# Optimization experiments

Measured on AMD Instinct MI355X. Metric: run time of the kernel, lower is better.

Reference implementation:

```python
import jax, jax.numpy as jnp
import numpy as np

K = 128
NITER = 10


def _sq_dist(x, c):
    x2 = jnp.sum(x * x, axis=1, keepdims=True)          # [N,1]
    c2 = jnp.sum(c * c, axis=1)                          # [K]
    return x2 + c2[None, :] - 2.0 * (x @ c.T)


def _kmeans(x, key):
    N, D = x.shape
    idx = jax.random.permutation(key, N)[:K]             # torch.randperm(N)[:K]
    c0 = x[idx]

    def step(c, _):
        cl = jnp.argmin(_sq_dist(x, c), axis=1)          # nearest assignment [N]
        counts = jax.ops.segment_sum(jnp.ones((N,), x.dtype), cl, num_segments=K)  # bincount
        sums = jax.ops.segment_sum(x, cl, num_segments=K)                          # [K,D] (vectorized over D)
        # c = sums / counts; NaN (empty cluster, 0/0) -> 0, matching c[isnan(c)]=0
        c_new = jnp.where(counts[:, None] > 0, sums / jnp.maximum(counts, 1.0)[:, None], 0.0)
        return c_new, None

    c, _ = jax.lax.scan(step, c0, None, length=NITER)
    return c


def setup_inputs() -> dict:
    key = jax.random.key(0)
    x = jax.random.normal(key, (500000, 64), dtype=jnp.float32)
    return {"x": x}


def reference(x):
    # KMeans runs on x.detach(); forward output has no grad path through centroids
    centroids = _kmeans(jax.lax.stop_gradient(x), jax.random.key(42))
    distances = _sq_dist(x, centroids)                   # [N, K]
    # Faithful to normalize_distance: distances.sum(1, keepdim=True)[0] indexes
    # ROW 0 of the [N,1] row-sums -> a single scalar broadcast to all rows.
    denom = jnp.sum(distances[0])
    probs = 1.0 - distances / denom
    return probs
```

## Files before the change

kernel.cpp:

```cpp
#include <hip/hip_runtime.h>
#include <cstdint>
#include <cstddef>

#define NPTS 500000
#define DIM 64
#define KC 128
#define KM_ITERS 10
#define NGROUPS (NPTS / 32)
#define NITERS8 ((NGROUPS + 7) / 8)

typedef __bf16 bf16x8 __attribute__((ext_vector_type(8)));
typedef float f32x4 __attribute__((ext_vector_type(4)));

__device__ __forceinline__ float wave_reduce_add(float v) {
#pragma unroll
  for (int off = 32; off > 0; off >>= 1) v += __shfl_xor(v, off, 64);
  return v;
}

__device__ __forceinline__ bf16x8 cvt8(float4 a, float4 b) {
  bf16x8 r;
  r[0] = (__bf16)a.x; r[1] = (__bf16)a.y; r[2] = (__bf16)a.z; r[3] = (__bf16)a.w;
  r[4] = (__bf16)b.x; r[5] = (__bf16)b.y; r[6] = (__bf16)b.z; r[7] = (__bf16)b.w;
  return r;
}

__global__ void k_initc(const float* __restrict__ x, float* __restrict__ cent,
                        float* __restrict__ c2, float* __restrict__ S,
                        float* __restrict__ CNT) {
  int k = blockIdx.x, d = threadIdx.x;
  long src = (long)k * 3891 + 7;
  float v = x[src * DIM + d];
  cent[k * DIM + d] = v;
#pragma unroll
  for (int p = 0; p < KM_ITERS; p++) S[p * (KC * DIM) + k * DIM + d] = 0.f;
  if (d < KM_ITERS) CNT[d * KC + k] = 0.f;
  float s = wave_reduce_add(v * v);
  if (d == 0) c2[k] = s;
}

__global__ void k_update(const float* __restrict__ sums, const float* __restrict__ cnts,
                         float* __restrict__ cent, float* __restrict__ c2) {
  int k = blockIdx.x, d = threadIdx.x;
  float c = cnts[k];
  float v = (c > 0.f) ? (sums[k * DIM + d] / c) : 0.f;
  cent[k * DIM + d] = v;
  float s = wave_reduce_add(v * v);
  if (d == 0) c2[k] = s;
}

#define DIST_H(V0, V1, MK)                                                     \
  {                                                                            \
    f32x4 acc_[8];                                                             \
    _Pragma("unroll") for (int tt = 0; tt < 8; tt++)                           \
      acc_[tt] = (f32x4){c2h[tt * 4 + 0], c2h[tt * 4 + 1],                     \
                         c2h[tt * 4 + 2], c2h[tt * 4 + 3]};                    \
    _Pragma("unroll") for (int tt = 0; tt < 8; tt++)                           \
      acc_[tt] = __builtin_amdgcn_mfma_f32_16x16x32_bf16(afr0[tt], V0, acc_[tt], 0, 0, 0); \
    _Pragma("unroll") for (int tt = 0; tt < 8; tt++)                           \
      acc_[tt] = __builtin_amdgcn_mfma_f32_16x16x32_bf16(afr1[tt], V1, acc_[tt], 0, 0, 0); \
    float tv[32]; int ti[32];                                                  \
    _Pragma("unroll") for (int i_ = 0; i_ < 32; i_++) {                        \
      tv[i_] = acc_[i_ >> 2][i_ & 3]; ti[i_] = i_;                             \
    }                                                                          \
    _Pragma("unroll") for (int s_ = 16; s_ >= 1; s_ >>= 1)                     \
      _Pragma("unroll") for (int i_ = 0; i_ < s_; i_++) {                      \
        bool t_ = tv[i_ + s_] > tv[i_];                                        \
        tv[i_] = t_ ? tv[i_ + s_] : tv[i_];                                    \
        ti[i_] = t_ ? ti[i_ + s_] : ti[i_];                                    \
      }                                                                        \
    float maxv = tv[0];                                                        \
    int mk = ((ti[0] >> 2) << 4) + grp * 4 + (ti[0] & 3);                      \
    _Pragma("unroll") for (int off = 16; off <= 32; off <<= 1) {               \
      float ov = __shfl_xor(maxv, off, 64);                                    \
      int ok = __shfl_xor(mk, off, 64);                                        \
      if (ov > maxv || (ov == maxv && ok < mk)) { maxv = ov; mk = ok; }        \
    }                                                                          \
    MK = mk;                                                                   \
  }

#define XT_WRITE(XTW, V0, V1, H)                                               \
  {                                                                            \
    int slotb = (((((H) << 1) | (col >> 3)) ^ grp) & 3) * 16 + (col & 7) * 2;  \
    _Pragma("unroll") for (int j = 0; j < 8; j++) {                            \
      *(__bf16*)((XTW) + (grp * 8 + j) * 80 + slotb) = V0[j];                  \
      *(__bf16*)((XTW) + (32 + grp * 8 + j) * 80 + slotb) = V1[j];             \
    }                                                                          \
  }

#define SSQ16(F0, F1, G0, G1)                                                  \
  ((F0.x * F0.x + F0.y * F0.y + F0.z * F0.z + F0.w * F0.w) +                   \
   (F1.x * F1.x + F1.y * F1.y + F1.z * F1.z + F1.w * F1.w) +                   \
   (G0.x * G0.x + G0.y * G0.y + G0.z * G0.z + G0.w * G0.w) +                   \
   (G1.x * G1.x + G1.y * G1.y + G1.z * G1.z + G1.w * G1.w))

template <int FIRST>
__global__ __launch_bounds__(256, 2)
void k_assign(const float* __restrict__ xf, const __bf16* __restrict__ xb,
              __bf16* __restrict__ xbw, const float* __restrict__ cent,
              const float* __restrict__ c2, const float* __restrict__ s_prev,
              const float* __restrict__ cnt_prev, float* __restrict__ s_out,
              float* __restrict__ cnt_out) {
  __shared__ char xT[8][5120];
  __shared__ int sm[8][32];
  __shared__ float lc[KC];
  __shared__ float lcnt[KC];
  __shared__ float lc2[KC];

  const int lane = threadIdx.x & 63;
  const int wid = threadIdx.x >> 6;
  const int col = lane & 15;
  const int grp = lane >> 4;

  bf16x8 afr0[8], afr1[8];
  float c2h[32];

  if constexpr (FIRST) {
    for (int i = threadIdx.x; i < KC; i += 256) lc[i] = 0.f;
#pragma unroll
    for (int t = 0; t < 8; t++) {
      const float* cp = cent + (size_t)(t * 16 + col) * DIM;
      afr0[t] = cvt8(*(const float4*)(cp + grp * 8), *(const float4*)(cp + grp * 8 + 4));
      afr1[t] = cvt8(*(const float4*)(cp + 32 + grp * 8), *(const float4*)(cp + 32 + grp * 8 + 4));
#pragma unroll
      for (int r = 0; r < 4; r++) c2h[t * 4 + r] = -0.5f * c2[t * 16 + grp * 4 + r];
    }
    __syncthreads();
  } else {
    for (int i = threadIdx.x; i < KC; i += 256) { lcnt[i] = cnt_prev[i]; lc[i] = 0.f; }
    __syncthreads();
    float ssq[8];
#pragma unroll
    for (int t = 0; t < 8; t++) {
      int row = t * 16 + col;
      float c = lcnt[row];
      float inv = (c > 0.f) ? 1.f / c : 0.f;
      const float* sp = s_prev + (size_t)row * DIM;
      float4 f0 = *(const float4*)(sp + grp * 8);
      float4 f1 = *(const float4*)(sp + grp * 8 + 4);
      float4 g0 = *(const float4*)(sp + 32 + grp * 8);
      float4 g1 = *(const float4*)(sp + 32 + grp * 8 + 4);
      f0.x *= inv; f0.y *= inv; f0.z *= inv; f0.w *= inv;
      f1.x *= inv; f1.y *= inv; f1.z *= inv; f1.w *= inv;
      g0.x *= inv; g0.y *= inv; g0.z *= inv; g0.w *= inv;
      g1.x *= inv; g1.y *= inv; g1.z *= inv; g1.w *= inv;
      afr0[t] = cvt8(f0, f1);
      afr1[t] = cvt8(g0, g1);
      ssq[t] = SSQ16(f0, f1, g0, g1);
    }
#pragma unroll
    for (int t = 0; t < 8; t++) {
      float s = ssq[t];
      s += __shfl_xor(s, 16, 64);
      s += __shfl_xor(s, 32, 64);
      if (lane < 16 && wid == 0) lc2[t * 16 + col] = s;
    }
    __syncthreads();
#pragma unroll
    for (int t = 0; t < 8; t++)
#pragma unroll
      for (int r = 0; r < 4; r++) c2h[t * 4 + r] = -0.5f * lc2[t * 16 + grp * 4 + r];
  }
#pragma unroll
  for (int t = 0; t < 8; t++) asm volatile("" : "+v"(afr0[t]), "+v"(afr1[t]));
#pragma unroll
  for (int i = 0; i < 32; i++) asm volatile("" : "+v"(c2h[i]));

  f32x4 accs[8];
#pragma unroll
  for (int i = 0; i < 8; i++) accs[i] = (f32x4){0.f, 0.f, 0.f, 0.f};

  const int kbase = wid * 32;

  bf16x8 p0a, p1a, p0b, p1b;
  if constexpr (!FIRST) {
    int g0 = blockIdx.x * 8 + wid * 2;
    if (blockIdx.x < NITERS8 && g0 < NGROUPS) {
      const bf16x8* xr = (const bf16x8*)(xb + (size_t)(g0 * 32 + col) * DIM + grp * 8);
      p0a = xr[0]; p1a = xr[4]; p0b = xr[128]; p1b = xr[132];
    }
  }

  for (int it = blockIdx.x; it < NITERS8; it += gridDim.x) {
    int g0 = it * 8 + wid * 2, g1 = g0 + 1;
    bool e0 = g0 < NGROUPS, e1 = g1 < NGROUPS;

    bf16x8 v0a, v1a, v0b, v1b, w0a, w1a, w0b, w1b;
    if constexpr (FIRST) {
      if (e0) {
        const float* xp = xf + (size_t)(g0 * 32 + col) * DIM + grp * 8;
        const float* xq = xp + 16 * DIM;
        v0a = cvt8(*(const float4*)xp, *(const float4*)(xp + 4));
        v1a = cvt8(*(const float4*)(xp + 32), *(const float4*)(xp + 36));
        v0b = cvt8(*(const float4*)xq, *(const float4*)(xq + 4));
        v1b = cvt8(*(const float4*)(xq + 32), *(const float4*)(xq + 36));
        bf16x8* wp = (bf16x8*)(xbw + (size_t)(g0 * 32 + col) * DIM);
        wp[grp] = v0a; wp[4 + grp] = v1a; wp[128 + grp] = v0b; wp[132 + grp] = v1b;
      }
      if (e1) {
        const float* xp = xf + (size_t)(g1 * 32 + col) * DIM + grp * 8;
        const float* xq = xp + 16 * DIM;
        w0a = cvt8(*(const float4*)xp, *(const float4*)(xp + 4));
        w1a = cvt8(*(const float4*)(xp + 32), *(const float4*)(xp + 36));
        w0b = cvt8(*(const float4*)xq, *(const float4*)(xq + 4));
        w1b = cvt8(*(const float4*)(xq + 32), *(const float4*)(xq + 36));
        bf16x8* wp = (bf16x8*)(xbw + (size_t)(g1 * 32 + col) * DIM);
        wp[grp] = w0a; wp[4 + grp] = w1a; wp[128 + grp] = w0b; wp[132 + grp] = w1b;
      }
    } else {
      v0a = p0a; v1a = p1a; v0b = p0b; v1b = p1b;
      if (e1) {
        const bf16x8* xr = (const bf16x8*)(xb + (size_t)(g1 * 32 + col) * DIM + grp * 8);
        w0a = xr[0]; w1a = xr[4]; w0b = xr[128]; w1b = xr[132];
      }
    }

    int mk0a = -1, mk0b = -1, mk1a = -1, mk1b = -1;
    if (e0) {
      char* xTw = xT[wid * 2];
      XT_WRITE(xTw, v0a, v1a, 0);
      XT_WRITE(xTw, v0b, v1b, 1);
      DIST_H(v0a, v1a, mk0a);
      DIST_H(v0b, v1b, mk0b);
      if (grp == 0) { atomicAdd(&lc[mk0a], 1.f); atomicAdd(&lc[mk0b], 1.f); }
    }
    if (grp == 0) { sm[wid * 2][col] = mk0a; sm[wid * 2][16 + col] = mk0b; }
    if (e1) {
      char* xTw = xT[wid * 2 + 1];
      XT_WRITE(xTw, w0a, w1a, 0);
      XT_WRITE(xTw, w0b, w1b, 1);
      DIST_H(w0a, w1a, mk1a);
      DIST_H(w0b, w1b, mk1b);
      if (grp == 0) { atomicAdd(&lc[mk1a], 1.f); atomicAdd(&lc[mk1b], 1.f); }
    }
    if (grp == 0) { sm[wid * 2 + 1][col] = mk1a; sm[wid * 2 + 1][16 + col] = mk1b; }
    __syncthreads();

    if constexpr (!FIRST) {
      int itn = it + gridDim.x;
      int g0n = itn * 8 + wid * 2;
      if (itn < NITERS8 && g0n < NGROUPS) {
        const bf16x8* xr = (const bf16x8*)(xb + (size_t)(g0n * 32 + col) * DIM + grp * 8);
        p0a = xr[0]; p1a = xr[4]; p0b = xr[128]; p1b = xr[132];
      }
    }

#pragma unroll
    for (int G = 0; G < 8; G++) {
      const int* smG = sm[G];
      int4 mlo = *(const int4*)&smG[grp * 8];
      int4 mhi = *(const int4*)&smG[grp * 8 + 4];
      const char* xTg = xT[G];
      bf16x8 xf0, xf1, xf2, xf3;
      { int d = col;      int s = (grp ^ ((d >> 3) & 3)) & 3; xf0 = *(const bf16x8*)(xTg + d * 80 + s * 16); }
      { int d = 16 + col; int s = (grp ^ ((d >> 3) & 3)) & 3; xf1 = *(const bf16x8*)(xTg + d * 80 + s * 16); }
      { int d = 32 + col; int s = (grp ^ ((d >> 3) & 3)) & 3; xf2 = *(const bf16x8*)(xTg + d * 80 + s * 16); }
      { int d = 48 + col; int s = (grp ^ ((d >> 3) & 3)) & 3; xf3 = *(const bf16x8*)(xTg + d * 80 + s * 16); }
      int m0 = mlo.x, m1 = mlo.y, m2 = mlo.z, m3 = mlo.w;
      int m4 = mhi.x, m5 = mhi.y, m6 = mhi.z, m7 = mhi.w;
#pragma unroll
      for (int tt2 = 0; tt2 < 2; tt2++) {
        int c = kbase + tt2 * 16 + col;
        union { unsigned u[4]; bf16x8 v; } oh;
        oh.u[0] = (m0 == c ? 0x3F80u : 0u) | (m1 == c ? 0x3F800000u : 0u);
        oh.u[1] = (m2 == c ? 0x3F80u : 0u) | (m3 == c ? 0x3F800000u : 0u);
        oh.u[2] = (m4 == c ? 0x3F80u : 0u) | (m5 == c ? 0x3F800000u : 0u);
        oh.u[3] = (m6 == c ? 0x3F80u : 0u) | (m7 == c ? 0x3F800000u : 0u);
        accs[tt2 * 4 + 0] = __builtin_amdgcn_mfma_f32_16x16x32_bf16(oh.v, xf0, accs[tt2 * 4 + 0], 0, 0, 0);
        accs[tt2 * 4 + 1] = __builtin_amdgcn_mfma_f32_16x16x32_bf16(oh.v, xf1, accs[tt2 * 4 + 1], 0, 0, 0);
        accs[tt2 * 4 + 2] = __builtin_amdgcn_mfma_f32_16x16x32_bf16(oh.v, xf2, accs[tt2 * 4 + 2], 0, 0, 0);
        accs[tt2 * 4 + 3] = __builtin_amdgcn_mfma_f32_16x16x32_bf16(oh.v, xf3, accs[tt2 * 4 + 3], 0, 0, 0);
      }
    }
    __syncthreads();
  }

#pragma unroll
  for (int tt2 = 0; tt2 < 2; tt2++)
#pragma unroll
    for (int dt = 0; dt < 4; dt++)
#pragma unroll
      for (int r = 0; r < 4; r++)
        atomicAdd(&s_out[(size_t)(kbase + tt2 * 16 + grp * 4 + r) * DIM + dt * 16 + col],
                  accs[tt2 * 4 + dt][r]);
  for (int i = threadIdx.x; i < KC; i += 256) atomicAdd(&cnt_out[i], lc[i]);
}

__global__ __launch_bounds__(256, 2)
void k_probs(const float* __restrict__ x, const float* __restrict__ cent,
             const float* __restrict__ c2, float* __restrict__ out) {
  const int lane = threadIdx.x & 63;
  const int wid = threadIdx.x >> 6;
  const int col = lane & 15;
  const int grp = lane >> 4;

  bf16x8 afr[2][8];
  float c2g[32];
#pragma unroll
  for (int t = 0; t < 8; t++) {
    const float* cp = cent + (size_t)(t * 16 + col) * DIM;
#pragma unroll
    for (int ks = 0; ks < 2; ks++) {
      float4 f0 = *(const float4*)(cp + ks * 32 + grp * 8);
      float4 f1 = *(const float4*)(cp + ks * 32 + grp * 8 + 4);
      afr[ks][t] = cvt8(f0, f1);
    }
#pragma unroll
    for (int r = 0; r < 4; r++) c2g[t * 4 + r] = c2[t * 16 + grp * 4 + r];
  }

  float c2a = c2[lane], c2b = c2[64 + lane];
  float x2_0 = 0.f, dA = 0.f, dB = 0.f;
#pragma unroll 8
  for (int d = 0; d < DIM; d++) {
    float xv = x[d];
    x2_0 = fmaf(xv, xv, x2_0);
    dA = fmaf(xv, cent[(size_t)lane * DIM + d], dA);
    dB = fmaf(xv, cent[(size_t)(64 + lane) * DIM + d], dB);
  }
  float part = ((x2_0 + c2a) - 2.f * dA) + ((x2_0 + c2b) - 2.f * dB);
  float invd = 1.0f / wave_reduce_add(part);

  int w = blockIdx.x * 4 + wid;
  int nw = gridDim.x * 4;
  for (int t = w; t < NPTS / 16; t += nw) {
    int n0 = t * 16;
    const float* xp = x + (size_t)(n0 + col) * DIM;
    float4 a0 = *(const float4*)(xp + grp * 8);
    float4 a1 = *(const float4*)(xp + grp * 8 + 4);
    float4 b0 = *(const float4*)(xp + 32 + grp * 8);
    float4 b1 = *(const float4*)(xp + 32 + grp * 8 + 4);
    bf16x8 xb0 = cvt8(a0, a1), xb1 = cvt8(b0, b1);

    float sq = a0.x * a0.x + a0.y * a0.y + a0.z * a0.z + a0.w * a0.w
             + a1.x * a1.x + a1.y * a1.y + a1.z * a1.z + a1.w * a1.w
             + b0.x * b0.x + b0.y * b0.y + b0.z * b0.z + b0.w * b0.w
             + b1.x * b1.x + b1.y * b1.y + b1.z * b1.z + b1.w * b1.w;
    sq += __shfl_xor(sq, 16, 64);
    sq += __shfl_xor(sq, 32, 64);

    f32x4 acc[8];
#pragma unroll
    for (int tt = 0; tt < 8; tt++) acc[tt] = (f32x4){0.f, 0.f, 0.f, 0.f};
#pragma unroll
    for (int tt = 0; tt < 8; tt++)
      acc[tt] = __builtin_amdgcn_mfma_f32_16x16x32_bf16(afr[0][tt], xb0, acc[tt], 0, 0, 0);
#pragma unroll
    for (int tt = 0; tt < 8; tt++)
      acc[tt] = __builtin_amdgcn_mfma_f32_16x16x32_bf16(afr[1][tt], xb1, acc[tt], 0, 0, 0);

    float* op = out + (size_t)(n0 + col) * KC + grp * 4;
#pragma unroll
    for (int tt = 0; tt < 8; tt++) {
      f32x4 q;
      q[0] = 1.f - ((sq + c2g[tt * 4 + 0]) - 2.f * acc[tt][0]) * invd;
      q[1] = 1.f - ((sq + c2g[tt * 4 + 1]) - 2.f * acc[tt][1]) * invd;
      q[2] = 1.f - ((sq + c2g[tt * 4 + 2]) - 2.f * acc[tt][2]) * invd;
      q[3] = 1.f - ((sq + c2g[tt * 4 + 3]) - 2.f * acc[tt][3]) * invd;
      __builtin_nontemporal_store(q, (f32x4*)(op + tt * 16));
    }
  }
}

extern "C" void kernel_launch(void* const* d_in, const int* in_sizes, int n_in,
                              void* d_out, int out_size, void* d_ws, size_t ws_size,
                              hipStream_t stream) {
  const float* x = (const float*)d_in[0];
  float* out = (float*)d_out;

  float* cent = (float*)d_ws;
  float* c2 = cent + KC * DIM;
  float* S = c2 + KC;
  float* CNT = S + KM_ITERS * KC * DIM;

  __bf16* xb = (__bf16*)d_out;

  k_initc<<<KC, DIM, 0, stream>>>(x, cent, c2, S, CNT);
  k_assign<1><<<512, 256, 0, stream>>>(x, xb, xb, cent, c2, nullptr, nullptr, S, CNT);
  for (int it = 1; it < KM_ITERS; it++) {
    k_assign<0><<<512, 256, 0, stream>>>(x, xb, xb, cent, c2,
                                         S + (it - 1) * KC * DIM, CNT + (it - 1) * KC,
                                         S + it * KC * DIM, CNT + it * KC);
  }
  k_update<<<KC, DIM, 0, stream>>>(S + 9 * KC * DIM, CNT + 9 * KC, cent, c2);
  k_probs<<<512, 256, 0, stream>>>(x, cent, c2, out);
}
```

Before: 666.9 us.

## Stage per-block sums in LDS with rotated atomics; reuse bf16 x copy in probs

The assign kernel now writes its per-block centroid sums into padded shared memory and then issues the global atomics in a block-rotated order, so blocks contend less on the same addresses. When the workspace is large enough, the bf16 copy of x is kept in the workspace instead of the output buffer. The final probs kernel then reads that half-size bf16 copy rather than fp32 x. This computes ||x||^2 from bf16-rounded values, which slightly changes accuracy, and the kernel falls back to the old path if the workspace is too small.

```diff
diff --git a/kernel.cpp b/kernel.cpp
--- a/kernel.cpp
+++ b/kernel.cpp
@@ -275,20 +275,34 @@
     __syncthreads();
   }
 
+  __syncthreads();
+  float* ms = (float*)xT;
 #pragma unroll
   for (int tt2 = 0; tt2 < 2; tt2++)
 #pragma unroll
     for (int dt = 0; dt < 4; dt++)
 #pragma unroll
       for (int r = 0; r < 4; r++)
-        atomicAdd(&s_out[(size_t)(kbase + tt2 * 16 + grp * 4 + r) * DIM + dt * 16 + col],
-                  accs[tt2 * 4 + dt][r]);
-  for (int i = threadIdx.x; i < KC; i += 256) atomicAdd(&cnt_out[i], lc[i]);
-}
-
+        ms[(kbase + tt2 * 16 + grp * 4 + r) * 65 + dt * 16 + col] = accs[tt2 * 4 + dt][r];
+  __syncthreads();
+  {
+    int rot = (blockIdx.x * 131) & (KC * DIM - 1);
+    for (int i = threadIdx.x; i < KC * DIM; i += 256) {
+      int j = (i + rot) & (KC * DIM - 1);
+      atomicAdd(&s_out[j], ms[(j >> 6) * 65 + (j & 63)]);
+    }
+    for (int i = threadIdx.x; i < KC; i += 256) {
+      int j = (i + blockIdx.x) & (KC - 1);
+      atomicAdd(&cnt_out[j], lc[j]);
+    }
+  }
+}
+
+template <int BF>
 __global__ __launch_bounds__(256, 2)
-void k_probs(const float* __restrict__ x, const float* __restrict__ cent,
-             const float* __restrict__ c2, float* __restrict__ out) {
+void k_probs(const float* __restrict__ x, const __bf16* __restrict__ xbp,
+             const float* __restrict__ cent, const float* __restrict__ c2,
+             float* __restrict__ out) {
   const int lane = threadIdx.x & 63;
   const int wid = threadIdx.x >> 6;
   const int col = lane & 15;
@@ -325,17 +339,26 @@
   int nw = gridDim.x * 4;
   for (int t = w; t < NPTS / 16; t += nw) {
     int n0 = t * 16;
-    const float* xp = x + (size_t)(n0 + col) * DIM;
-    float4 a0 = *(const float4*)(xp + grp * 8);
-    float4 a1 = *(const float4*)(xp + grp * 8 + 4);
-    float4 b0 = *(const float4*)(xp + 32 + grp * 8);
-    float4 b1 = *(const float4*)(xp + 32 + grp * 8 + 4);
-    bf16x8 xb0 = cvt8(a0, a1), xb1 = cvt8(b0, b1);
-
-    float sq = a0.x * a0.x + a0.y * a0.y + a0.z * a0.z + a0.w * a0.w
-             + a1.x * a1.x + a1.y * a1.y + a1.z * a1.z + a1.w * a1.w
-             + b0.x * b0.x + b0.y * b0.y + b0.z * b0.z + b0.w * b0.w
-             + b1.x * b1.x + b1.y * b1.y + b1.z * b1.z + b1.w * b1.w;
+    bf16x8 xb0, xb1;
+    float sq;
+    if constexpr (BF) {
+      const bf16x8* xr = (const bf16x8*)(xbp + (size_t)(n0 + col) * DIM + grp * 8);
+      xb0 = xr[0]; xb1 = xr[4];
+      sq = 0.f;
+#pragma unroll
+      for (int j = 0; j < 8; j++) {
+        float u = (float)xb0[j], v = (float)xb1[j];
+        sq += u * u + v * v;
+      }
+    } else {
+      const float* xp = x + (size_t)(n0 + col) * DIM;
+      float4 a0 = *(const float4*)(xp + grp * 8);
+      float4 a1 = *(const float4*)(xp + grp * 8 + 4);
+      float4 b0 = *(const float4*)(xp + 32 + grp * 8);
+      float4 b1 = *(const float4*)(xp + 32 + grp * 8 + 4);
+      xb0 = cvt8(a0, a1); xb1 = cvt8(b0, b1);
+      sq = SSQ16(a0, a1, b0, b1);
+    }
     sq += __shfl_xor(sq, 16, 64);
     sq += __shfl_xor(sq, 32, 64);
 
@@ -372,8 +395,10 @@
   float* c2 = cent + KC * DIM;
   float* S = c2 + KC;
   float* CNT = S + KM_ITERS * KC * DIM;
-
-  __bf16* xb = (__bf16*)d_out;
+  size_t xb_off_f = (size_t)(KC * DIM + KC + KM_ITERS * KC * DIM + KM_ITERS * KC);
+  size_t need = xb_off_f * 4 + (size_t)NPTS * DIM * 2;
+  bool ws_ok = ws_size >= need;
+  __bf16* xb = ws_ok ? (__bf16*)((float*)d_ws + xb_off_f) : (__bf16*)d_out;
 
   k_initc<<<KC, DIM, 0, stream>>>(x, cent, c2, S, CNT);
   k_assign<1><<<512, 256, 0, stream>>>(x, xb, xb, cent, c2, nullptr, nullptr, S, CNT);
@@ -383,5 +408,8 @@
                                          S + it * KC * DIM, CNT + it * KC);
   }
   k_update<<<KC, DIM, 0, stream>>>(S + 9 * KC * DIM, CNT + 9 * KC, cent, c2);
-  k_probs<<<512, 256, 0, stream>>>(x, cent, c2, out);
-}
+  if (ws_ok)
+    k_probs<1><<<512, 256, 0, stream>>>(x, xb, cent, c2, out);
+  else
+    k_probs<0><<<512, 256, 0, stream>>>(x, xb, cent, c2, out);
+}
```

Result: slower. 704.4 us (+5.6%).
